# Performance work log

Measured on AMD Instinct MI355X. Metric: run time of the kernel, lower is better.

The kernel has to match this reference:

```python
import jax, jax.numpy as jnp
import numpy as np

BER = 0.02          # ber_curve.ber_at(snr_db) evaluated at snr_db=10
BITS = 9            # ceil(log2(512)) for both coarse and fine codebooks
KC = 512
KF = 512
B, HC, WC, HF, WF, D = 64, 32, 32, 64, 64, 128


def _bitflip_channel(idx, u, bits, K):
    """Pack->bitflip->unpack->clip, vectorized.

    LSB-first packing of exactly bits-per-symbol means flipping bits of the
    packed byte stream == flipping each symbol's `bits` bits independently
    (flipped padding bits in the final byte are discarded by unpack).
    idx: [...] int32, u: [..., bits] float32 uniform(0,1).
    """
    shifts = jnp.arange(bits, dtype=jnp.int32)
    bitmat = (idx[..., None] >> shifts) & 1                       # [..., bits]
    flips = (u < BER).astype(jnp.int32)
    bitmat = jnp.bitwise_xor(bitmat, flips)
    rx = jnp.sum(bitmat << shifts, axis=-1)                       # [...]
    return jnp.clip(rx, 0, K - 1)


def setup_inputs() -> dict:
    key = jax.random.key(0)
    k1, k2, k3, k4, k5, k6 = jax.random.split(key, 6)
    return {
        "idx_c": jax.random.randint(k1, (B, HC, WC), 0, KC, dtype=jnp.int32),
        "idx_f": jax.random.randint(k2, (B, HF, WF), 0, KF, dtype=jnp.int32),
        "codebook_c": jax.random.normal(k3, (KC, D), dtype=jnp.float32),
        "codebook_f": jax.random.normal(k4, (KF, D), dtype=jnp.float32),
        "flip_u_c": jax.random.uniform(k5, (B, HC, WC, BITS), dtype=jnp.float32),
        "flip_u_f": jax.random.uniform(k6, (B, HF, WF, BITS), dtype=jnp.float32),
    }


def reference(idx_c, idx_f, codebook_c, codebook_f, flip_u_c, flip_u_f):
    rx_c = _bitflip_channel(idx_c, flip_u_c, BITS, KC)            # [B,Hc,Wc]
    rx_f = _bitflip_channel(idx_f, flip_u_f, BITS, KF)            # [B,Hf,Wf]
    # indices_to_quantized: embedding gather from each codebook
    q_coarse = codebook_c[rx_c]                                   # [B,Hc,Wc,D]
    q_fine = codebook_f[rx_f]                                     # [B,Hf,Wf,D]
    b = q_fine.shape[0]
    out = jnp.concatenate(
        [q_fine.reshape(b, -1), q_coarse.reshape(b, -1)], axis=1
    )
    return out
```

## Files before the change

kernel.cpp:

```cpp
#include <hip/hip_runtime.h>


constexpr int   BITS       = 9;
constexpr float BER        = 0.02f;
constexpr int   Bn         = 64;
constexpr int   HC = 32, WC = 32, HF = 64, WF = 64, D = 128;
constexpr int   NF         = Bn * HF * WF;
constexpr int   NC         = Bn * HC * WC;
constexpr int   NTOT       = NF + NC;
constexpr int   FINE_ROW   = HF * WF * D;
constexpr int   COARSE_ROW = HC * WC * D;
constexpr int   ROW        = FINE_ROW + COARSE_ROW;

__global__ __launch_bounds__(256) void chan_gather_kernel(
    const int*   __restrict__ idx_c,
    const int*   __restrict__ idx_f,
    const float* __restrict__ cb_c,
    const float* __restrict__ cb_f,
    const float* __restrict__ u_c,
    const float* __restrict__ u_f,
    float*       __restrict__ out)
{
    __shared__ int s_row[8];
    __shared__ int s_off[8];
    __shared__ int s_coarse[8];

    const int t   = threadIdx.x;
    const int blk = blockIdx.x;

    if (t < 8) {
        const int i = blk * 8 + t;
        int v, off, coarse;
        const float* u;
        if (i < NF) {
            const int b   = i >> 12;
            const int rem = i & 4095;
            off    = b * ROW + rem * D;
            v      = idx_f[i];
            u      = u_f + (size_t)i * BITS;
            coarse = 0;
        } else {
            const int j   = i - NF;
            const int b   = j >> 10;
            const int rem = j & 1023;
            off    = b * ROW + FINE_ROW + rem * D;
            v      = idx_c[j];
            u      = u_c + (size_t)j * BITS;
            coarse = 1;
        }
        int flip = 0;
        #pragma unroll
        for (int k = 0; k < BITS; ++k)
            flip |= (u[k] < BER) ? (1 << k) : 0;
        s_row[t]    = (v ^ flip) & 511;
        s_off[t]    = off;
        s_coarse[t] = coarse;
    }
    __syncthreads();

    const int g    = t >> 5;
    const int lane = t & 31;
    const float* cb = s_coarse[g] ? cb_c : cb_f;
    const float4 val = ((const float4*)(cb + s_row[g] * D))[lane];
    ((float4*)(out + s_off[g]))[lane] = val;
}

extern "C" void kernel_launch(void* const* d_in, const int* in_sizes, int n_in,
                              void* d_out, int out_size, void* d_ws, size_t ws_size,
                              hipStream_t stream) {
    const int*   idx_c = (const int*)  d_in[0];
    const int*   idx_f = (const int*)  d_in[1];
    const float* cb_c  = (const float*)d_in[2];
    const float* cb_f  = (const float*)d_in[3];
    const float* u_c   = (const float*)d_in[4];
    const float* u_f   = (const float*)d_in[5];
    float*       out   = (float*)d_out;

    chan_gather_kernel<<<NTOT / 8, 256, 0, stream>>>(
        idx_c, idx_f, cb_c, cb_f, u_c, u_f, out);
}
```

Before: 199.5 us.

## Use persistent grid with wave ballot for bit flips, drop shared memory sync

The kernel now launches a fixed grid of 2048 blocks that loop over symbols instead of one block per 8 symbols. Each 32-lane group computes its symbol's flip mask in parallel, with lanes loading one uniform each and a wave ballot building the mask. This replaces the serial 9-load loop in 8 threads followed by a shared-memory barrier. It aims to cut launch and block-scheduling overhead and the serialized latency before the gather. The cost is redundant index and branch computation in every lane, and it relies on the 64-wide wavefront layout holding two symbols per wave.

New measurement: 204.3 us. 2.4% more time.

```diff
diff --git a/kernel.cpp b/kernel.cpp
--- a/kernel.cpp
+++ b/kernel.cpp
@@ -12,6 +12,10 @@
 constexpr int   COARSE_ROW = HC * WC * D;
 constexpr int   ROW        = FINE_ROW + COARSE_ROW;
 
+constexpr int   GRID  = 2048;
+constexpr int   SYMS_PER_BLK_ITER = 8;
+constexpr int   ITERS = NTOT / (SYMS_PER_BLK_ITER * GRID);
+
 __global__ __launch_bounds__(256) void chan_gather_kernel(
     const int*   __restrict__ idx_c,
     const int*   __restrict__ idx_f,
@@ -21,48 +25,42 @@
     const float* __restrict__ u_f,
     float*       __restrict__ out)
 {
-    __shared__ int s_row[8];
-    __shared__ int s_off[8];
-    __shared__ int s_coarse[8];
+    const int t          = threadIdx.x;
+    const int sym_in_blk = t >> 5;
+    const int half       = (t >> 5) & 1;
+    const int lane32     = t & 31;
 
-    const int t   = threadIdx.x;
-    const int blk = blockIdx.x;
+    #pragma unroll
+    for (int it = 0; it < ITERS; ++it) {
+        const int c = it * GRID + blockIdx.x;
+        const int i = c * SYMS_PER_BLK_ITER + sym_in_blk;
 
-    if (t < 8) {
-        const int i = blk * 8 + t;
-        int v, off, coarse;
-        const float* u;
+        const float* u;  const int* idxp;  const float* cb;
+        int off, local;
         if (i < NF) {
-            const int b   = i >> 12;
-            const int rem = i & 4095;
-            off    = b * ROW + rem * D;
-            v      = idx_f[i];
-            u      = u_f + (size_t)i * BITS;
-            coarse = 0;
+            const int b = i >> 12, rem = i & 4095;
+            off   = b * ROW + rem * D;
+            u     = u_f;  idxp = idx_f;  cb = cb_f;
+            local = i;
         } else {
-            const int j   = i - NF;
-            const int b   = j >> 10;
-            const int rem = j & 1023;
-            off    = b * ROW + FINE_ROW + rem * D;
-            v      = idx_c[j];
-            u      = u_c + (size_t)j * BITS;
-            coarse = 1;
+            const int j = i - NF;
+            const int b = j >> 10, rem = j & 1023;
+            off   = b * ROW + FINE_ROW + rem * D;
+            u     = u_c;  idxp = idx_c;  cb = cb_c;
+            local = j;
         }
-        int flip = 0;
-        #pragma unroll
-        for (int k = 0; k < BITS; ++k)
-            flip |= (u[k] < BER) ? (1 << k) : 0;
-        s_row[t]    = (v ^ flip) & 511;
-        s_off[t]    = off;
-        s_coarse[t] = coarse;
+
+        bool pred = false;
+        if (lane32 < BITS)
+            pred = u[(size_t)local * BITS + lane32] < BER;
+        const unsigned long long m = __ballot(pred);
+        const int flip = (int)((m >> (half << 5)) & 511u);
+
+        const int row = (idxp[local] ^ flip) & 511;
+
+        const float4 val = ((const float4*)(cb + row * D))[lane32];
+        ((float4*)(out + off))[lane32] = val;
     }
-    __syncthreads();
-
-    const int g    = t >> 5;
-    const int lane = t & 31;
-    const float* cb = s_coarse[g] ? cb_c : cb_f;
-    const float4 val = ((const float4*)(cb + s_row[g] * D))[lane];
-    ((float4*)(out + s_off[g]))[lane] = val;
 }
 
 extern "C" void kernel_launch(void* const* d_in, const int* in_sizes, int n_in,
@@ -76,6 +74,6 @@
     const float* u_f   = (const float*)d_in[5];
     float*       out   = (float*)d_out;
 
-    chan_gather_kernel<<<NTOT / 8, 256, 0, stream>>>(
+    chan_gather_kernel<<<GRID, 256, 0, stream>>>(
         idx_c, idx_f, cb_c, cb_f, u_c, u_f, out);
 }
```
